# Kernel optimization log

Hardware: AMD Instinct MI355X
Metric: run time of the kernel (lower is better)

Reference implementation:

```python
import jax, jax.numpy as jnp
import numpy as np

N, H, W = 4096, 96, 96
C0 = 0.28209479177387814
C1 = 0.4886025119029199
C2 = [1.0925484305920792, -1.0925484305920792, 0.31539156525252005, -1.0925484305920792, 0.5462742152960396]
C3 = [-0.5900435899266435, 2.890611442640554, -0.4570457994644658, 0.3731763325901154, -0.4570457994644658, 1.445305721320277, -0.5900435899266435]


def setup_inputs() -> dict:
    key = jax.random.key(0)
    ks = jax.random.split(key, 6)
    return {
        'pws': jax.random.normal(ks[0], (N, 3), jnp.float32),
        'low_shs': 0.5 * jax.random.normal(ks[1], (N, 3), jnp.float32),
        'high_shs': 0.1 * jax.random.normal(ks[2], (N, 45), jnp.float32),
        'alphas_raw': jax.random.normal(ks[3], (N, 1), jnp.float32),
        'scales_raw': 0.5 * jax.random.normal(ks[4], (N, 3), jnp.float32) - 3.0,
        'rots_raw': jax.random.normal(ks[5], (N, 4), jnp.float32),
        'us': jnp.zeros((N, 2), jnp.float32),
        'Rcw': jnp.eye(3, dtype=jnp.float32),
        'tcw': jnp.array([0.0, 0.0, 4.0], jnp.float32),
        'cam_intr': jnp.array([120.0, 120.0, 48.0, 48.0], jnp.float32),  # fx fy cx cy
    }


def quat_to_rot(q):
    w, x, y, z = q[:, 0], q[:, 1], q[:, 2], q[:, 3]
    return jnp.stack([
        jnp.stack([1 - 2 * (y * y + z * z), 2 * (x * y - w * z), 2 * (x * z + w * y)], -1),
        jnp.stack([2 * (x * y + w * z), 1 - 2 * (x * x + z * z), 2 * (y * z - w * x)], -1),
        jnp.stack([2 * (x * z - w * y), 2 * (y * z + w * x), 1 - 2 * (x * x + y * y)], -1),
    ], -2)  # [N,3,3]


def sh2color(shs, dirs):
    # shs [N,16,3], dirs [N,3] normalized view directions
    x, y, z = dirs[:, 0:1], dirs[:, 1:2], dirs[:, 2:3]
    xx, yy, zz = x * x, y * y, z * z
    xy, yz, xz = x * y, y * z, x * z
    c = C0 * shs[:, 0]
    c = c - C1 * y * shs[:, 1] + C1 * z * shs[:, 2] - C1 * x * shs[:, 3]
    c = (c + C2[0] * xy * shs[:, 4] + C2[1] * yz * shs[:, 5]
         + C2[2] * (2 * zz - xx - yy) * shs[:, 6]
         + C2[3] * xz * shs[:, 7] + C2[4] * (xx - yy) * shs[:, 8])
    c = (c + C3[0] * y * (3 * xx - yy) * shs[:, 9] + C3[1] * xy * z * shs[:, 10]
         + C3[2] * y * (4 * zz - xx - yy) * shs[:, 11]
         + C3[3] * z * (2 * zz - 3 * xx - 3 * yy) * shs[:, 12]
         + C3[4] * x * (4 * zz - xx - yy) * shs[:, 13]
         + C3[5] * z * (xx - yy) * shs[:, 14]
         + C3[6] * x * (xx - 3 * yy) * shs[:, 15])
    return jnp.maximum(c + 0.5, 0.0)  # [N,3]


def _forward(pws, low_shs, high_shs, alphas_raw, scales_raw, rots_raw, Rcw, tcw, cam_intr):
    fx, fy, cx, cy = cam_intr[0], cam_intr[1], cam_intr[2], cam_intr[3]
    alphas = jax.nn.sigmoid(alphas_raw)[:, 0]                 # get_alphas
    scales = jnp.exp(scales_raw)                              # get_scales
    rots = rots_raw / jnp.linalg.norm(rots_raw, axis=1, keepdims=True)  # get_rots
    shs = jnp.concatenate([low_shs, high_shs], axis=1).reshape(-1, 16, 3)

    # --- project ---
    pcs = pws @ Rcw.T + tcw                                   # [N,3] camera coords
    depths = pcs[:, 2]
    zs = jnp.where(depths > 1e-6, depths, 1e-6)
    u = jnp.stack([fx * pcs[:, 0] / zs + cx, fy * pcs[:, 1] / zs + cy], axis=1)

    # --- cov3d = (R S)(R S)^T ---
    M = quat_to_rot(rots) * scales[:, None, :]
    cov3d = M @ jnp.swapaxes(M, 1, 2)                          # [N,3,3]

    # --- cov2d = J W cov3d W^T J^T + 0.3 I ---
    limx, limy = 1.3 * (W / (2.0 * fx)), 1.3 * (H / (2.0 * fy))
    tx = jnp.clip(pcs[:, 0] / zs, -limx, limx) * zs
    ty = jnp.clip(pcs[:, 1] / zs, -limy, limy) * zs
    zero = jnp.zeros_like(zs)
    J = jnp.stack([
        jnp.stack([fx / zs, zero, -fx * tx / (zs * zs)], -1),
        jnp.stack([zero, fy / zs, -fy * ty / (zs * zs)], -1),
    ], -2)                                                     # [N,2,3]
    T = J @ Rcw
    cov2d = T @ cov3d @ jnp.swapaxes(T, 1, 2)
    a = cov2d[:, 0, 0] + 0.3
    b = cov2d[:, 0, 1]
    c2 = cov2d[:, 1, 1] + 0.3

    # --- inverseCov2D + areas (radius of 3-sigma ellipse) ---
    det = a * c2 - b * b
    cinv = jnp.stack([c2, -b, a], axis=1) / det[:, None]       # [N,3]
    mid = 0.5 * (a + c2)
    lam = mid + jnp.sqrt(jnp.maximum(mid * mid - det, 0.1))
    radius = jnp.ceil(3.0 * jnp.sqrt(lam))
    areas = jnp.stack([radius, radius], axis=1)                # [N,2]

    # --- sh2Color ---
    twc = -(Rcw.T @ tcw)
    dirs = pws - twc
    dirs = dirs / jnp.linalg.norm(dirs, axis=1, keepdims=True)
    colors = sh2color(shs, dirs)                               # [N,3]

    # --- splat: depth-sorted alpha compositing ---
    valid = depths > 0.2
    order = jnp.argsort(depths)
    u_s, cinv_s = u[order], cinv[order]
    alpha_s, color_s, valid_s = alphas[order], colors[order], valid[order]

    px = (jnp.arange(W, dtype=jnp.float32))[None, :].repeat(H, 0).reshape(-1)
    py = (jnp.arange(H, dtype=jnp.float32))[:, None].repeat(W, 1).reshape(-1)
    dx = u_s[:, 0:1] - px[None, :]                             # [N,P]
    dy = u_s[:, 1:2] - py[None, :]
    power = -0.5 * (cinv_s[:, 0:1] * dx * dx + cinv_s[:, 2:3] * dy * dy) - cinv_s[:, 1:2] * dx * dy
    ap = jnp.minimum(alpha_s[:, None] * jnp.exp(jnp.minimum(power, 0.0)), 0.99)
    ap = jnp.where((ap >= 1.0 / 255.0) & valid_s[:, None], ap, 0.0)
    logt = jnp.cumsum(jnp.log1p(-ap), axis=0)
    tau = jnp.exp(jnp.concatenate([jnp.zeros((1, ap.shape[1])), logt[:-1]], axis=0))
    wgt = jnp.where(tau > 1e-4, ap * tau, 0.0)                 # [N,P]
    image = jnp.einsum('nc,np->cp', color_s, wgt).reshape(3, H, W)
    return image, areas


def reference(pws, low_shs, high_shs, alphas_raw, scales_raw, rots_raw, us, Rcw, tcw, cam_intr):
    return _forward(pws, low_shs, high_shs, alphas_raw, scales_raw, rots_raw, Rcw, tcw, cam_intr)
```

## Files before the change

### kernel.cpp

```cpp
#include <hip/hip_runtime.h>
#include <hip/hip_bf16.h>
#include <math.h>

#define GS_N 4096
#define IMG_H 96
#define IMG_W 96
#define NPIX (IMG_H * IMG_W)
#define TILE_PX 12
#define TILES_X 8
#define NTILES (TILES_X * TILES_X)
#define WAVES_PER_TILE 36

#define SH_C0 0.28209479177387814f
#define SH_C1 0.4886025119029199f
__device__ __constant__ float kC2[5] = {1.0925484305920792f, -1.0925484305920792f, 0.31539156525252005f, -1.0925484305920792f, 0.5462742152960396f};
__device__ __constant__ float kC3[7] = {-0.5900435899266435f, 2.890611442640554f, -0.4570457994644658f, 0.3731763325901154f, -0.4570457994644658f, 1.445305721320277f, -0.5900435899266435f};

__global__ __launch_bounds__(256) void gs_prep(
    const float* __restrict__ pws, const float* __restrict__ low_shs,
    const float* __restrict__ high_shs, const float* __restrict__ alphas_raw,
    const float* __restrict__ scales_raw, const float* __restrict__ rots_raw,
    const float* __restrict__ Rcw, const float* __restrict__ tcw,
    const float* __restrict__ cam,
    float* __restrict__ areas_out,
    float* __restrict__ depth_ws,
    int*   __restrict__ rank_ws,
    float4* __restrict__ A_uns,
    float4* __restrict__ B_uns,
    float* __restrict__ C_uns,
    float4* __restrict__ D_uns,
    unsigned long long* __restrict__ mask_ws)
{
    int i = blockIdx.x * 256 + threadIdx.x;
    if (i >= GS_N) return;

    rank_ws[i] = 0;
    mask_ws[i] = 0ull;

    float fx = cam[0], fy = cam[1], cxi = cam[2], cyi = cam[3];
    float R0 = Rcw[0], R1 = Rcw[1], R2 = Rcw[2];
    float R3 = Rcw[3], R4 = Rcw[4], R5 = Rcw[5];
    float R6 = Rcw[6], R7 = Rcw[7], R8 = Rcw[8];
    float t0 = tcw[0], t1 = tcw[1], t2 = tcw[2];

    float pwx = pws[3*i+0], pwy = pws[3*i+1], pwz = pws[3*i+2];

    float pcx = R0*pwx + R1*pwy + R2*pwz + t0;
    float pcy = R3*pwx + R4*pwy + R5*pwz + t1;
    float pcz = R6*pwx + R7*pwy + R8*pwz + t2;

    float depth = pcz;
    float zs = (depth > 1e-6f) ? depth : 1e-6f;

    float ux = fx * pcx / zs + cxi;
    float uy = fy * pcy / zs + cyi;

    float alpha = 1.0f / (1.0f + expf(-alphas_raw[i]));

    float s0 = expf(scales_raw[3*i+0]);
    float s1 = expf(scales_raw[3*i+1]);
    float s2 = expf(scales_raw[3*i+2]);

    float qw = rots_raw[4*i+0], qx = rots_raw[4*i+1], qy = rots_raw[4*i+2], qz = rots_raw[4*i+3];
    float qn = sqrtf(qw*qw + qx*qx + qy*qy + qz*qz);
    qw /= qn; qx /= qn; qy /= qn; qz /= qn;

    float r00 = 1.0f - 2.0f*(qy*qy + qz*qz);
    float r01 = 2.0f*(qx*qy - qw*qz);
    float r02 = 2.0f*(qx*qz + qw*qy);
    float r10 = 2.0f*(qx*qy + qw*qz);
    float r11 = 1.0f - 2.0f*(qx*qx + qz*qz);
    float r12 = 2.0f*(qy*qz - qw*qx);
    float r20 = 2.0f*(qx*qz - qw*qy);
    float r21 = 2.0f*(qy*qz + qw*qx);
    float r22 = 1.0f - 2.0f*(qx*qx + qy*qy);

    float m00 = r00*s0, m01 = r01*s1, m02 = r02*s2;
    float m10 = r10*s0, m11 = r11*s1, m12 = r12*s2;
    float m20 = r20*s0, m21 = r21*s1, m22 = r22*s2;

    float V00 = m00*m00 + m01*m01 + m02*m02;
    float V01 = m00*m10 + m01*m11 + m02*m12;
    float V02 = m00*m20 + m01*m21 + m02*m22;
    float V11 = m10*m10 + m11*m11 + m12*m12;
    float V12 = m10*m20 + m11*m21 + m12*m22;
    float V22 = m20*m20 + m21*m21 + m22*m22;

    float limx = 1.3f * ((float)IMG_W / (2.0f * fx));
    float limy = 1.3f * ((float)IMG_H / (2.0f * fy));
    float xzr = pcx / zs, yzr = pcy / zs;
    float txv = fminf(fmaxf(xzr, -limx), limx) * zs;
    float tyv = fminf(fmaxf(yzr, -limy), limy) * zs;

    float J00 = fx / zs, J02 = -fx * txv / (zs * zs);
    float J11 = fy / zs, J12 = -fy * tyv / (zs * zs);

    float T00 = J00*R0 + J02*R6, T01 = J00*R1 + J02*R7, T02 = J00*R2 + J02*R8;
    float T10 = J11*R3 + J12*R6, T11 = J11*R4 + J12*R7, T12 = J11*R5 + J12*R8;

    float TW00 = T00*V00 + T01*V01 + T02*V02;
    float TW01 = T00*V01 + T01*V11 + T02*V12;
    float TW02 = T00*V02 + T01*V12 + T02*V22;
    float TW10 = T10*V00 + T11*V01 + T12*V02;
    float TW11 = T10*V01 + T11*V11 + T12*V12;
    float TW12 = T10*V02 + T11*V12 + T12*V22;

    float c00 = TW00*T00 + TW01*T01 + TW02*T02;
    float c01 = TW00*T10 + TW01*T11 + TW02*T12;
    float c11 = TW10*T10 + TW11*T11 + TW12*T12;

    float a  = c00 + 0.3f;
    float b  = c01;
    float cc = c11 + 0.3f;
    float det = a * cc - b * b;
    float ci0 = cc / det;
    float ci1 = -b / det;
    float ci2 = a / det;

    float mid = 0.5f * (a + cc);
    float lam = mid + sqrtf(fmaxf(mid * mid - det, 0.1f));
    float radius = ceilf(3.0f * sqrtf(lam));
    areas_out[2*i + 0] = radius;
    areas_out[2*i + 1] = radius;

    float twcx = -(R0*t0 + R3*t1 + R6*t2);
    float twcy = -(R1*t0 + R4*t1 + R7*t2);
    float twcz = -(R2*t0 + R5*t1 + R8*t2);
    float dx = pwx - twcx, dy = pwy - twcy, dz = pwz - twcz;
    float dn = sqrtf(dx*dx + dy*dy + dz*dz);
    dx /= dn; dy /= dn; dz /= dn;

    float xx = dx*dx, yy = dy*dy, zz = dz*dz;
    float xy = dx*dy, yz = dy*dz, xz = dx*dz;

    float bas0  = SH_C0;
    float bas1  = -SH_C1 * dy;
    float bas2  =  SH_C1 * dz;
    float bas3  = -SH_C1 * dx;
    float bas4  = kC2[0] * xy;
    float bas5  = kC2[1] * yz;
    float bas6  = kC2[2] * (2.0f*zz - xx - yy);
    float bas7  = kC2[3] * xz;
    float bas8  = kC2[4] * (xx - yy);
    float bas9  = kC3[0] * dy * (3.0f*xx - yy);
    float bas10 = kC3[1] * xy * dz;
    float bas11 = kC3[2] * dy * (4.0f*zz - xx - yy);
    float bas12 = kC3[3] * dz * (2.0f*zz - 3.0f*xx - 3.0f*yy);
    float bas13 = kC3[4] * dx * (4.0f*zz - xx - yy);
    float bas14 = kC3[5] * dz * (xx - yy);
    float bas15 = kC3[6] * dx * (xx - 3.0f*yy);

    float col[3];
    #pragma unroll
    for (int c = 0; c < 3; ++c) {
        const float* hs = high_shs + 45*i + c;
        float acc = bas0 * low_shs[3*i + c];
        acc += bas1  * hs[0*3];
        acc += bas2  * hs[1*3];
        acc += bas3  * hs[2*3];
        acc += bas4  * hs[3*3];
        acc += bas5  * hs[4*3];
        acc += bas6  * hs[5*3];
        acc += bas7  * hs[6*3];
        acc += bas8  * hs[7*3];
        acc += bas9  * hs[8*3];
        acc += bas10 * hs[9*3];
        acc += bas11 * hs[10*3];
        acc += bas12 * hs[11*3];
        acc += bas13 * hs[12*3];
        acc += bas14 * hs[13*3];
        acc += bas15 * hs[14*3];
        col[c] = fmaxf(acc + 0.5f, 0.0f);
    }

    bool valid = depth > 0.2f;
    float al_eff = valid ? alpha : 0.0f;

    float Tthr = __logf(255.0f * al_eff) + 1e-4f;
    float rx = (Tthr > 0.0f) ? sqrtf(2.0f * Tthr * a)  : -1.0f;
    float ry = (Tthr > 0.0f) ? sqrtf(2.0f * Tthr * cc) : -1.0f;

    depth_ws[i] = depth;
    A_uns[i] = make_float4(ux, uy, ci0, ci1);
    B_uns[i] = make_float4(ci2, al_eff, col[0], col[1]);
    C_uns[i] = col[2];
    D_uns[i] = make_float4(ux, uy, rx, ry);
}

__global__ __launch_bounds__(256) void gs_rank_partial(
    const float* __restrict__ depth, int* __restrict__ rank_ws)
{
    __shared__ float sd[256];
    int itile = blockIdx.x >> 4;
    int jtile = blockIdx.x & 15;
    int tid = threadIdx.x;
    int i = itile * 256 + tid;

    sd[tid] = depth[jtile * 256 + tid];
    __syncthreads();

    float mg = depth[i];
    int jbase = jtile * 256;
    int rank = 0;
    const float4* s4 = (const float4*)sd;
    #pragma unroll 16
    for (int jj = 0; jj < 64; ++jj) {
        float4 v = s4[jj];
        int j0 = jbase + jj * 4;
        rank += (v.x < mg || (v.x == mg && (j0+0) < i)) ? 1 : 0;
        rank += (v.y < mg || (v.y == mg && (j0+1) < i)) ? 1 : 0;
        rank += (v.z < mg || (v.z == mg && (j0+2) < i)) ? 1 : 0;
        rank += (v.w < mg || (v.w == mg && (j0+3) < i)) ? 1 : 0;
    }
    atomicAdd(&rank_ws[i], rank);
}

__global__ __launch_bounds__(256) void gs_gather_mask(
    const int* __restrict__ rank_ws,
    const float4* __restrict__ A_uns, const float4* __restrict__ B_uns,
    const float* __restrict__ C_uns, const float4* __restrict__ D_uns,
    float4* __restrict__ A_s, float4* __restrict__ B_s, float* __restrict__ C_s,
    unsigned long long* __restrict__ mask_ws)
{
    int i = blockIdx.x * 256 + threadIdx.x;
    int r = rank_ws[i];
    A_s[r] = A_uns[i];
    B_s[r] = B_uns[i];
    C_s[r] = C_uns[i];

    float4 d = D_uns[i];
    if (d.z >= 0.0f) {
        const float inv = 1.0f / (float)TILE_PX;
        int tx0 = max(0, (int)ceilf((d.x - d.z - (float)(TILE_PX - 1)) * inv - 1e-4f));
        int tx1 = min(TILES_X - 1, (int)floorf((d.x + d.z) * inv + 1e-4f));
        int ty0 = max(0, (int)ceilf((d.y - d.w - (float)(TILE_PX - 1)) * inv - 1e-4f));
        int ty1 = min(TILES_X - 1, (int)floorf((d.y + d.w) * inv + 1e-4f));
        unsigned long long bit = 1ull << (r & 63);
        int w = r >> 6;
        for (int ty = ty0; ty <= ty1; ++ty)
            for (int tx = tx0; tx <= tx1; ++tx)
                atomicOr(&mask_ws[(ty * TILES_X + tx) * 64 + w], bit);
    }
}

__global__ __launch_bounds__(256) void gs_raster(
    const float4* __restrict__ A_s, const float4* __restrict__ B_s,
    const float* __restrict__ C_s,
    const unsigned long long* __restrict__ mask_ws,
    float* __restrict__ img)
{
    __shared__ unsigned short slist[GS_N];
    __shared__ int scnt;

    int b = blockIdx.x;
    int tile = b / WAVES_PER_TILE;
    int sub  = b - tile * WAVES_PER_TILE;
    int lane = threadIdx.x & 63;
    int wv   = threadIdx.x >> 6;

    if (wv == 0) {
        unsigned long long m = mask_ws[tile * 64 + lane];
        int c = __popcll(m);
        int incl = c;
        #pragma unroll
        for (int d = 1; d < 64; d <<= 1) {
            int v = __shfl_up(incl, d, 64);
            if (lane >= d) incl += v;
        }
        int off = incl - c;
        int base = lane << 6;
        while (m) {
            int bpos = __builtin_ctzll(m);
            m &= m - 1;
            slist[off++] = (unsigned short)(base + bpos);
        }
        if (lane == 63) scnt = incl;
    }
    __syncthreads();
    int cnt = scnt;

    int idxp = sub * 4 + wv;
    int lx = idxp % TILE_PX, ly = idxp / TILE_PX;
    int tx = tile & (TILES_X - 1), ty = tile >> 3;
    int pxi = tx * TILE_PX + lx, pyi = ty * TILE_PX + ly;
    float px = (float)pxi, py = (float)pyi;
    int p = pyi * IMG_W + pxi;

    float carry = 1.0f;
    float accr = 0.0f, accg = 0.0f, accb = 0.0f;

    for (int c0 = 0; c0 < cnt; c0 += 64) {
        int k = c0 + lane;
        float ap = 0.0f, colr = 0.0f, colg = 0.0f, colb = 0.0f;
        if (k < cnt) {
            int n = slist[k];
            float4 a4 = A_s[n];
            float4 b4 = B_s[n];
            colb = C_s[n];
            colr = b4.z; colg = b4.w;

            float ddx = a4.x - px;
            float ddy = a4.y - py;
            float pw = -0.5f * (a4.z * ddx * ddx + b4.x * ddy * ddy) - a4.w * ddx * ddy;
            pw = fminf(pw, 0.0f);
            ap = b4.y * __expf(pw);
            ap = fminf(ap, 0.99f);
            ap = (ap >= (1.0f / 255.0f)) ? ap : 0.0f;
        }

        if (__ballot(ap > 0.0f) == 0ull) continue;

        float f = 1.0f - ap;
        float incl = f;
        #pragma unroll
        for (int d = 1; d < 64; d <<= 1) {
            float v = __shfl_up(incl, d, 64);
            if (lane >= d) incl *= v;
        }
        float excl = __shfl_up(incl, 1, 64);
        if (lane == 0) excl = 1.0f;

        float tau = carry * excl;
        float wgt = (tau > 1e-4f) ? ap * tau : 0.0f;
        accr += colr * wgt;
        accg += colg * wgt;
        accb += colb * wgt;

        carry *= __shfl(incl, 63, 64);
        if (carry <= 1e-4f) break;
    }

    #pragma unroll
    for (int d = 32; d >= 1; d >>= 1) {
        accr += __shfl_xor(accr, d, 64);
        accg += __shfl_xor(accg, d, 64);
        accb += __shfl_xor(accb, d, 64);
    }
    if (lane == 0) {
        img[0 * NPIX + p] = accr;
        img[1 * NPIX + p] = accg;
        img[2 * NPIX + p] = accb;
    }
}

extern "C" void kernel_launch(void* const* d_in, const int* in_sizes, int n_in,
                              void* d_out, int out_size, void* d_ws, size_t ws_size,
                              hipStream_t stream) {
    const float* pws        = (const float*)d_in[0];
    const float* low_shs    = (const float*)d_in[1];
    const float* high_shs   = (const float*)d_in[2];
    const float* alphas_raw = (const float*)d_in[3];
    const float* scales_raw = (const float*)d_in[4];
    const float* rots_raw   = (const float*)d_in[5];
    const float* Rcw        = (const float*)d_in[7];
    const float* tcw        = (const float*)d_in[8];
    const float* cam        = (const float*)d_in[9];

    float* out_img   = (float*)d_out;
    float* out_areas = (float*)d_out + 3 * NPIX;

    char* ws = (char*)d_ws;
    float*  depth_ws = (float*) (ws + 0);
    int*    rank_ws  = (int*)   (ws + 16384);
    float4* A_uns    = (float4*)(ws + 32768);
    float4* B_uns    = (float4*)(ws + 98304);
    float*  C_uns    = (float*) (ws + 163840);
    float4* D_uns    = (float4*)(ws + 180224);
    float4* A_s      = (float4*)(ws + 245760);
    float4* B_s      = (float4*)(ws + 311296);
    float*  C_s      = (float*) (ws + 376832);
    unsigned long long* mask_ws = (unsigned long long*)(ws + 393216);

    gs_prep<<<GS_N / 256, 256, 0, stream>>>(
        pws, low_shs, high_shs, alphas_raw, scales_raw, rots_raw, Rcw, tcw, cam,
        out_areas, depth_ws, rank_ws, A_uns, B_uns, C_uns, D_uns, mask_ws);

    gs_rank_partial<<<256, 256, 0, stream>>>(depth_ws, rank_ws);

    gs_gather_mask<<<GS_N / 256, 256, 0, stream>>>(
        rank_ws, A_uns, B_uns, C_uns, D_uns, A_s, B_s, C_s, mask_ws);

    gs_raster<<<NTILES * WAVES_PER_TILE, 256, 0, stream>>>(
        A_s, B_s, C_s, mask_ws, out_img);
}
```

Measured before the change: 96.26 us.

## Precompute per-tile compacted gaussian lists in a separate expand kernel

Adds a gs_expand kernel that builds each tile's compacted gaussian index list once and gathers the A/B/C attributes into contiguous per-tile buffers. gs_raster then reads those buffers with coalesced loads instead of having every block rebuild the bitmask list and do indirect gathers. The cost is an extra kernel launch, more workspace (about 9 MB), and an extra write-then-read round trip through global memory.

```diff
diff --git a/kernel.cpp b/kernel.cpp
--- a/kernel.cpp
+++ b/kernel.cpp
@@ -243,20 +243,19 @@
     }
 }
 
-__global__ __launch_bounds__(256) void gs_raster(
+__global__ __launch_bounds__(256) void gs_expand(
+    const unsigned long long* __restrict__ mask_ws,
     const float4* __restrict__ A_s, const float4* __restrict__ B_s,
     const float* __restrict__ C_s,
-    const unsigned long long* __restrict__ mask_ws,
-    float* __restrict__ img)
+    float4* __restrict__ E_A, float4* __restrict__ E_B, float* __restrict__ E_C,
+    int* __restrict__ tile_cnt)
 {
     __shared__ unsigned short slist[GS_N];
     __shared__ int scnt;
 
-    int b = blockIdx.x;
-    int tile = b / WAVES_PER_TILE;
-    int sub  = b - tile * WAVES_PER_TILE;
-    int lane = threadIdx.x & 63;
-    int wv   = threadIdx.x >> 6;
+    int tile = blockIdx.x;
+    int tid = threadIdx.x;
+    int lane = tid & 63, wv = tid >> 6;
 
     if (wv == 0) {
         unsigned long long m = mask_ws[tile * 64 + lane];
@@ -274,10 +273,33 @@
             m &= m - 1;
             slist[off++] = (unsigned short)(base + bpos);
         }
-        if (lane == 63) scnt = incl;
+        if (lane == 63) { scnt = incl; tile_cnt[tile] = incl; }
     }
     __syncthreads();
     int cnt = scnt;
+
+    float4* tA = E_A + tile * GS_N;
+    float4* tB = E_B + tile * GS_N;
+    float*  tC = E_C + tile * GS_N;
+    for (int k = tid; k < cnt; k += 256) {
+        int n = slist[k];
+        tA[k] = A_s[n];
+        tB[k] = B_s[n];
+        tC[k] = C_s[n];
+    }
+}
+
+__global__ __launch_bounds__(256) void gs_raster(
+    const float4* __restrict__ E_A, const float4* __restrict__ E_B,
+    const float* __restrict__ E_C,
+    const int* __restrict__ tile_cnt,
+    float* __restrict__ img)
+{
+    int b = blockIdx.x;
+    int tile = b / WAVES_PER_TILE;
+    int sub  = b - tile * WAVES_PER_TILE;
+    int lane = threadIdx.x & 63;
+    int wv   = threadIdx.x >> 6;
 
     int idxp = sub * 4 + wv;
     int lx = idxp % TILE_PX, ly = idxp / TILE_PX;
@@ -286,6 +308,11 @@
     float px = (float)pxi, py = (float)pyi;
     int p = pyi * IMG_W + pxi;
 
+    int cnt = tile_cnt[tile];
+    const float4* tA = E_A + tile * GS_N;
+    const float4* tB = E_B + tile * GS_N;
+    const float*  tC = E_C + tile * GS_N;
+
     float carry = 1.0f;
     float accr = 0.0f, accg = 0.0f, accb = 0.0f;
 
@@ -293,10 +320,9 @@
         int k = c0 + lane;
         float ap = 0.0f, colr = 0.0f, colg = 0.0f, colb = 0.0f;
         if (k < cnt) {
-            int n = slist[k];
-            float4 a4 = A_s[n];
-            float4 b4 = B_s[n];
-            colb = C_s[n];
+            float4 a4 = tA[k];
+            float4 b4 = tB[k];
+            colb = tC[k];
             colr = b4.z; colg = b4.w;
 
             float ddx = a4.x - px;
@@ -370,6 +396,10 @@
     float4* B_s      = (float4*)(ws + 311296);
     float*  C_s      = (float*) (ws + 376832);
     unsigned long long* mask_ws = (unsigned long long*)(ws + 393216);
+    float4* E_A      = (float4*)(ws + 425984);
+    float4* E_B      = (float4*)(ws + 4620288);
+    float*  E_C      = (float*) (ws + 8814592);
+    int*    tile_cnt = (int*)   (ws + 9863168);
 
     gs_prep<<<GS_N / 256, 256, 0, stream>>>(
         pws, low_shs, high_shs, alphas_raw, scales_raw, rots_raw, Rcw, tcw, cam,
@@ -380,6 +410,9 @@
     gs_gather_mask<<<GS_N / 256, 256, 0, stream>>>(
         rank_ws, A_uns, B_uns, C_uns, D_uns, A_s, B_s, C_s, mask_ws);
 
+    gs_expand<<<NTILES, 256, 0, stream>>>(
+        mask_ws, A_s, B_s, C_s, E_A, E_B, E_C, tile_cnt);
+
     gs_raster<<<NTILES * WAVES_PER_TILE, 256, 0, stream>>>(
-        A_s, B_s, C_s, mask_ws, out_img);
-}
+        E_A, E_B, E_C, tile_cnt, out_img);
+}
```

Result: no change. 95.05 us (-1.3%).
